# Optimization experiments

Hardware: AMD Instinct MI355X
Metric: run time of the kernel (lower is better)

## Reference

```python
import jax, jax.numpy as jnp
import numpy as np

B, S, D, H = 2, 2048, 1024, 16
HD = D // H  # 64


def setup_inputs() -> dict:
    key = jax.random.key(0)
    ks = jax.random.split(key, 7)
    s = 1.0 / np.sqrt(HD)
    return {
        "x": jax.random.normal(ks[0], (B, S, D), dtype=jnp.float32),
        "Wq": jax.random.normal(ks[1], (H, HD, HD), dtype=jnp.float32) * s,
        "bq": jax.random.normal(ks[2], (H, HD), dtype=jnp.float32) * 0.01,
        "Wk": jax.random.normal(ks[3], (H, HD, HD), dtype=jnp.float32) * s,
        "bk": jax.random.normal(ks[4], (H, HD), dtype=jnp.float32) * 0.01,
        "Wv": jax.random.normal(ks[5], (H, HD, HD), dtype=jnp.float32) * s,
        "bv": jax.random.normal(ks[6], (H, HD), dtype=jnp.float32) * 0.01,
    }


def reference(x, Wq, bq, Wk, bk, Wv, bv):
    b, s, d = x.shape
    h, hd, _ = Wq.shape
    # Faithful to torch: x.view(B, H, S, hd) is a raw reshape (mixes seq positions
    # across heads), NOT a transpose-based head split.
    xh = x.reshape(b, h, s, hd)
    # torch Linear: y @ W.T + b, with W of shape (out, in)
    q = jnp.einsum('bhse,hde->bhsd', xh, Wq) + bq[None, :, None, :]
    k = jnp.einsum('bhse,hde->bhsd', xh, Wk) + bk[None, :, None, :]
    v = jnp.einsum('bhse,hde->bhsd', xh, Wv) + bv[None, :, None, :]
    scale = 1.0 / jnp.sqrt(jnp.asarray(d / h, dtype=jnp.float32))
    attn = jax.nn.softmax(jnp.einsum('bhqd,bhkd->bhqk', q, k) * scale, axis=-1)
    out = jnp.einsum('bhqk,bhkd->bhqd', attn, v)
    # torch.cat over heads along last dim == transpose then merge
    return out.transpose(0, 2, 1, 3).reshape(b, s, d)
```

## Files before the change

### kernel.cpp

```cpp
#include <hip/hip_runtime.h>
#include <hip/hip_bf16.h>

#define BATCH 2
#define SEQ   2048
#define DMODEL 1024
#define NH    16
#define HD    64
#define QSCALE 0.1803368801111602f

typedef __attribute__((ext_vector_type(8))) short bf16x8;
typedef __attribute__((ext_vector_type(4))) float f32x4;

__device__ __forceinline__ ushort f2bf(float f) {
    union { float f; unsigned u; } v; v.f = f;
    return (ushort)((v.u + 0x8000u) >> 16);
}

__device__ __forceinline__ unsigned pack2bf(float a, float b) {
    union { float f; unsigned u; } x, y; x.f = a; y.f = b;
    return __builtin_amdgcn_perm(y.u + 0x8000u, x.u + 0x8000u, 0x07060302u);
}

__device__ __forceinline__ float exp2r(float x) {
#if __has_builtin(__builtin_amdgcn_exp2f)
    return __builtin_amdgcn_exp2f(x);
#else
    return exp2f(x);
#endif
}

__device__ __forceinline__ void g2l16(const void* g, void* l) {
    __builtin_amdgcn_global_load_lds(
        (const __attribute__((address_space(1))) unsigned*)g,
        (__attribute__((address_space(3))) unsigned*)l, 16, 0, 0);
}

#define MFMA(a, b, c) __builtin_amdgcn_mfma_f32_16x16x32_bf16((a), (b), (c), 0, 0, 0)

__global__ __launch_bounds__(256) void wfmt_kernel(
    const float* __restrict__ Wq, const float* __restrict__ Wk,
    const float* __restrict__ Wv, ushort* __restrict__ Wf)
{
    const int blk = blockIdx.x;
    const int h = blk / 3, m = blk - h * 3;
    const float* W = (m == 0 ? Wq : (m == 1 ? Wk : Wv)) + h * 4096;
    const float s = (m == 0) ? QSCALE : 1.0f;
    for (int i = 0; i < 2; ++i) {
        int idx = threadIdx.x + 256 * i;
        int l = idx & 63, chunk = idx >> 6;
        int qd = l >> 4, l16 = l & 15, nt = chunk >> 1, ks = chunk & 1;
        const float* src = W + (nt * 16 + l16) * 64 + ks * 32 + qd * 8;
        float4 a = *(const float4*)src;
        float4 b = *(const float4*)(src + 4);
        union { bf16x8 v; unsigned u[4]; } t;
        t.u[0] = pack2bf(a.x * s, a.y * s);
        t.u[1] = pack2bf(a.z * s, a.w * s);
        t.u[2] = pack2bf(b.x * s, b.y * s);
        t.u[3] = pack2bf(b.z * s, b.w * s);
        *(bf16x8*)&Wf[((size_t)blk * 512 + idx) * 8] = t.v;
    }
}

__global__ __launch_bounds__(256) void qkv_kernel(
    const float* __restrict__ x, const ushort* __restrict__ Wf,
    const float* __restrict__ bq, const float* __restrict__ bk,
    const float* __restrict__ bv,
    ushort* __restrict__ Qo, ushort* __restrict__ Kf, ushort* __restrict__ Vf)
{
    const int bid = blockIdx.x;
    const int st  = bid & 31;
    const int bh  = bid >> 5;
    const int h   = bh & (NH - 1);

    __shared__ ushort EbQ[64 * 72];
    __shared__ ushort EbK[64 * 72];
    __shared__ ushort EbV[64 * 72];

    const int tid  = threadIdx.x;
    const int wave = tid >> 6, lane = tid & 63;
    const int ln16 = lane & 15, quad = lane >> 4;

    const float* xr = x + (size_t)bh * (SEQ * HD)
                        + ((size_t)st * 64 + wave * 16 + ln16) * HD;
    bf16x8 afr[2];
#pragma unroll
    for (int ks = 0; ks < 2; ++ks) {
        const float4* p = (const float4*)(xr + ks * 32 + quad * 8);
        float4 a = p[0], b = p[1];
        union { bf16x8 v; unsigned u[4]; } t;
        t.u[0] = pack2bf(a.x, a.y);
        t.u[1] = pack2bf(a.z, a.w);
        t.u[2] = pack2bf(b.x, b.y);
        t.u[3] = pack2bf(b.z, b.w);
        afr[ks] = t.v;
    }

    const bf16x8* wf = (const bf16x8*)Wf + (size_t)h * 1536 + lane;

    f32x4 acc[3][4];
#pragma unroll
    for (int m = 0; m < 3; ++m)
#pragma unroll
        for (int nt = 0; nt < 4; ++nt) {
            f32x4 a = {0.f, 0.f, 0.f, 0.f};
            a = MFMA(afr[0], wf[(m * 8 + nt * 2 + 0) * 64], a);
            a = MFMA(afr[1], wf[(m * 8 + nt * 2 + 1) * 64], a);
            acc[m][nt] = a;
        }

#pragma unroll
    for (int nt = 0; nt < 4; ++nt) {
        float bbq = bq[h * 64 + nt * 16 + ln16] * QSCALE;
        float bbk = bk[h * 64 + nt * 16 + ln16];
#pragma unroll
        for (int r = 0; r < 4; ++r) {
            EbQ[(wave * 16 + quad * 4 + r) * 72 + nt * 16 + ln16] = f2bf(acc[0][nt][r] + bbq);
            EbK[(wave * 16 + quad * 4 + r) * 72 + nt * 16 + ln16] = f2bf(acc[1][nt][r] + bbk);
        }
        float bbv = bv[h * 64 + nt * 16 + ln16];
        ushort4 o;
        o.x = f2bf(acc[2][nt][0] + bbv);
        o.y = f2bf(acc[2][nt][1] + bbv);
        o.z = f2bf(acc[2][nt][2] + bbv);
        o.w = f2bf(acc[2][nt][3] + bbv);
        *(ushort4*)&EbV[(nt * 16 + ln16) * 72 + wave * 16 + quad * 4] = o;
    }
    __syncthreads();

    {
        ushort* dst = Qo + (size_t)bh * SEQ * HD + (size_t)st * 64 * HD;
        for (int i = 0; i < 2; ++i) {
            int idx = tid + 256 * i;
            int row = idx >> 3, c8 = (idx & 7) * 8;
            *(bf16x8*)&dst[row * 64 + c8] = *(const bf16x8*)&EbQ[row * 72 + c8];
        }
    }
    {
        ushort* dstK = Kf + ((size_t)bh * 32 + st) * 4096;
        ushort* dstV = Vf + ((size_t)bh * 32 + st) * 4096;
        for (int i = 0; i < 2; ++i) {
            int idx8 = tid + 256 * i;
            int l2 = idx8 & 63, chunk = idx8 >> 6;
            int nt = chunk >> 1, ks = chunk & 1;
            int qd = l2 >> 4, l16 = l2 & 15;
            *(bf16x8*)&dstK[(size_t)idx8 * 8] =
                *(const bf16x8*)&EbK[(nt * 16 + l16) * 72 + ks * 32 + qd * 8];
            *(bf16x8*)&dstV[(size_t)idx8 * 8] =
                *(const bf16x8*)&EbV[(nt * 16 + l16) * 72 + ks * 32 + qd * 8];
        }
    }
}

__global__ __launch_bounds__(256, 2) void attn_kernel(
    const ushort* __restrict__ Q, const ushort* __restrict__ Kf,
    const ushort* __restrict__ Vf, float* __restrict__ out)
{
    const int bid = blockIdx.x;
    const int wid = (bid & 7) * 64 + (bid >> 3);
    const int qt  = wid & 15;
    const int bh  = wid >> 4;
    const int h   = bh & (NH - 1), b = bh >> 4;

    __shared__ ushort Ksh[3][4096];
    __shared__ ushort Vsh[3][4096];
    __shared__ ushort Ps[4][2][2048];

    const int tid = threadIdx.x, wave = tid >> 6, lane = tid & 63;
    const int ln16 = lane & 15, quad = lane >> 4;
    const unsigned swz = (unsigned)(ln16 & 7) << 4;

    const char* kgb = (const char*)Kf + (size_t)bh * 32 * 8192 + wave * 2048 + lane * 16;
    const char* vgb = (const char*)Vf + (size_t)bh * 32 * 8192 + wave * 2048 + lane * 16;

    auto stage = [&](int kt, int sb) {
        const char* kg = kgb + (size_t)kt * 8192;
        const char* vg = vgb + (size_t)kt * 8192;
        ushort* kl = &Ksh[sb][wave * 1024];
        ushort* vl = &Vsh[sb][wave * 1024];
        g2l16(kg,        kl);
        g2l16(kg + 1024, kl + 512);
        g2l16(vg,        vl);
        g2l16(vg + 1024, vl + 512);
    };

    stage(0, 0);
    stage(1, 1);

    bf16x8 qfr[2][2];
#pragma unroll
    for (int g = 0; g < 2; ++g) {
        const ushort* Qg = Q + ((size_t)bh * SEQ + qt * 128 + wave * 32 + g * 16 + ln16) * HD;
        qfr[g][0] = *(const bf16x8*)&Qg[quad * 8];
        qfr[g][1] = *(const bf16x8*)&Qg[32 + quad * 8];
    }

    float lsum[2] = {0.f, 0.f};
    f32x4 accO[2][4];
#pragma unroll
    for (int g = 0; g < 2; ++g)
#pragma unroll
        for (int nt = 0; nt < 4; ++nt) accO[g][nt] = (f32x4){0.f, 0.f, 0.f, 0.f};

    bf16x8 vf[8];

    for (int kt = 0; kt < 32; ++kt) {
        const int cur = kt & 1;
        const int sb  = kt % 3;

        if (kt < 31) {
            asm volatile("s_waitcnt vmcnt(4)" ::: "memory");
        } else {
            asm volatile("s_waitcnt vmcnt(0)" ::: "memory");
        }
        __builtin_amdgcn_s_barrier();
        __builtin_amdgcn_sched_barrier(0);

        const ushort* Kb = &Ksh[sb][0];
        bf16x8 kf[8];
#pragma unroll
        for (int c = 0; c < 8; ++c) kf[c] = *(const bf16x8*)&Kb[c * 512 + lane * 8];

        f32x4 sacc[2][4];
        __builtin_amdgcn_s_setprio(1);
#pragma unroll
        for (int nt = 0; nt < 4; ++nt)
#pragma unroll
            for (int g = 0; g < 2; ++g) {
                f32x4 a = {0.f, 0.f, 0.f, 0.f};
                a = MFMA(kf[nt * 2],     qfr[g][0], a);
                a = MFMA(kf[nt * 2 + 1], qfr[g][1], a);
                sacc[g][nt] = a;
            }
        __builtin_amdgcn_s_setprio(0);

        if (kt > 0) {
            const char* Pr = (const char*)Ps[wave][1 - cur];
            bf16x8 pf[2][2];
#pragma unroll
            for (int g = 0; g < 2; ++g) {
                const char* Prr = Pr + (g * 16 + ln16) * 128;
                pf[g][0] = *(const bf16x8*)(Prr + (((unsigned)(quad * 16)) ^ swz));
                pf[g][1] = *(const bf16x8*)(Prr + (((unsigned)(64 + quad * 16)) ^ swz));
            }
            __builtin_amdgcn_s_setprio(1);
#pragma unroll
            for (int nt = 0; nt < 4; ++nt)
#pragma unroll
                for (int g = 0; g < 2; ++g) {
                    accO[g][nt] = MFMA(vf[nt * 2],     pf[g][0], accO[g][nt]);
                    accO[g][nt] = MFMA(vf[nt * 2 + 1], pf[g][1], accO[g][nt]);
                }
            __builtin_amdgcn_s_setprio(0);
        }

        const ushort* Vb = &Vsh[sb][0];
#pragma unroll
        for (int c = 0; c < 8; ++c) vf[c] = *(const bf16x8*)&Vb[c * 512 + lane * 8];

        char* Pw = (char*)Ps[wave][cur];
#pragma unroll
        for (int g = 0; g < 2; ++g) {
            char* Pwr = Pw + (g * 16 + ln16) * 128;
            float rs = 0.f;
#pragma unroll
            for (int nt = 0; nt < 4; ++nt) {
                float p0 = exp2r(sacc[g][nt][0]);
                float p1 = exp2r(sacc[g][nt][1]);
                float p2 = exp2r(sacc[g][nt][2]);
                float p3 = exp2r(sacc[g][nt][3]);
                rs += (p0 + p1) + (p2 + p3);
                uint2 pk;
                pk.x = pack2bf(p0, p1);
                pk.y = pack2bf(p2, p3);
                *(uint2*)(Pwr + (((unsigned)(nt * 32 + quad * 8)) ^ swz)) = pk;
            }
            lsum[g] += rs;
        }

        if (kt < 30) {
            asm volatile("s_waitcnt lgkmcnt(0)" ::: "memory");
            __builtin_amdgcn_sched_barrier(0);
            stage(kt + 2, (kt + 2) % 3);
        }
    }

    {
        const char* Pr = (const char*)Ps[wave][1];
        bf16x8 pf[2][2];
#pragma unroll
        for (int g = 0; g < 2; ++g) {
            const char* Prr = Pr + (g * 16 + ln16) * 128;
            pf[g][0] = *(const bf16x8*)(Prr + (((unsigned)(quad * 16)) ^ swz));
            pf[g][1] = *(const bf16x8*)(Prr + (((unsigned)(64 + quad * 16)) ^ swz));
        }
#pragma unroll
        for (int nt = 0; nt < 4; ++nt)
#pragma unroll
            for (int g = 0; g < 2; ++g) {
                accO[g][nt] = MFMA(vf[nt * 2],     pf[g][0], accO[g][nt]);
                accO[g][nt] = MFMA(vf[nt * 2 + 1], pf[g][1], accO[g][nt]);
            }
    }

#pragma unroll
    for (int g = 0; g < 2; ++g) {
        float l = lsum[g];
        l += __shfl_xor(l, 16, 64);
        l += __shfl_xor(l, 32, 64);
        float rinv = 1.0f / l;
        float* ob = out + ((size_t)b * SEQ + qt * 128 + wave * 32 + g * 16 + ln16) * DMODEL + h * HD;
#pragma unroll
        for (int nt = 0; nt < 4; ++nt) {
            float4 o;
            o.x = accO[g][nt][0] * rinv;
            o.y = accO[g][nt][1] * rinv;
            o.z = accO[g][nt][2] * rinv;
            o.w = accO[g][nt][3] * rinv;
            *(float4*)&ob[nt * 16 + quad * 4] = o;
        }
    }
}

extern "C" void kernel_launch(void* const* d_in, const int* in_sizes, int n_in,
                              void* d_out, int out_size, void* d_ws, size_t ws_size,
                              hipStream_t stream) {
    const float* x  = (const float*)d_in[0];
    const float* Wq = (const float*)d_in[1];
    const float* bq = (const float*)d_in[2];
    const float* Wk = (const float*)d_in[3];
    const float* bk = (const float*)d_in[4];
    const float* Wv = (const float*)d_in[5];
    const float* bv = (const float*)d_in[6];

    const size_t nElem = (size_t)BATCH * NH * SEQ * HD;
    ushort* Qw  = (ushort*)d_ws;
    ushort* Kw  = Qw + nElem;
    ushort* Vw  = Kw + nElem;
    ushort* Wfw = Vw + nElem;

    wfmt_kernel<<<48, 256, 0, stream>>>(Wq, Wk, Wv, Wfw);
    qkv_kernel<<<32 * 32, 256, 0, stream>>>(
        x, Wfw, bq, bk, bv, Qw, Kw, Vw);
    attn_kernel<<<BATCH * NH * (SEQ / 128), 256, 0, stream>>>(
        Qw, Kw, Vw, (float*)d_out);
}
```

Before: 132.5 us.

## Split attention KV range across two wave groups, load K/V directly to registers

The attention kernel now launches 512 threads per block. Two groups of four waves each process half of the 32 key tiles for the same query rows, and their partial outputs and row sums are combined through shared memory at the end. The LDS triple-buffered K/V staging with barriers is removed, and each wave loads K/V fragments straight from global memory into registers, prefetching the next K tile. This removes per-tile barriers and doubles parallelism per query tile. In exchange it relies on cache hits for repeated K/V reads across waves and adds a final reduction step.

```diff
diff --git a/kernel.cpp b/kernel.cpp
--- a/kernel.cpp
+++ b/kernel.cpp
@@ -27,12 +27,6 @@
 #else
     return exp2f(x);
 #endif
-}
-
-__device__ __forceinline__ void g2l16(const void* g, void* l) {
-    __builtin_amdgcn_global_load_lds(
-        (const __attribute__((address_space(1))) unsigned*)g,
-        (__attribute__((address_space(3))) unsigned*)l, 16, 0, 0);
 }
 
 #define MFMA(a, b, c) __builtin_amdgcn_mfma_f32_16x16x32_bf16((a), (b), (c), 0, 0, 0)
@@ -151,7 +145,7 @@
     }
 }
 
-__global__ __launch_bounds__(256, 2) void attn_kernel(
+__global__ __launch_bounds__(512, 4) void attn_kernel(
     const ushort* __restrict__ Q, const ushort* __restrict__ Kf,
     const ushort* __restrict__ Vf, float* __restrict__ out)
 {
@@ -161,39 +155,24 @@
     const int bh  = wid >> 4;
     const int h   = bh & (NH - 1), b = bh >> 4;
 
-    __shared__ ushort Ksh[3][4096];
-    __shared__ ushort Vsh[3][4096];
-    __shared__ ushort Ps[4][2][2048];
+    __shared__ ushort Ps[8][2][2048];
 
     const int tid = threadIdx.x, wave = tid >> 6, lane = tid & 63;
     const int ln16 = lane & 15, quad = lane >> 4;
+    const int qw = wave & 3, kh = wave >> 2;
     const unsigned swz = (unsigned)(ln16 & 7) << 4;
 
-    const char* kgb = (const char*)Kf + (size_t)bh * 32 * 8192 + wave * 2048 + lane * 16;
-    const char* vgb = (const char*)Vf + (size_t)bh * 32 * 8192 + wave * 2048 + lane * 16;
-
-    auto stage = [&](int kt, int sb) {
-        const char* kg = kgb + (size_t)kt * 8192;
-        const char* vg = vgb + (size_t)kt * 8192;
-        ushort* kl = &Ksh[sb][wave * 1024];
-        ushort* vl = &Vsh[sb][wave * 1024];
-        g2l16(kg,        kl);
-        g2l16(kg + 1024, kl + 512);
-        g2l16(vg,        vl);
-        g2l16(vg + 1024, vl + 512);
-    };
-
-    stage(0, 0);
-    stage(1, 1);
-
     bf16x8 qfr[2][2];
 #pragma unroll
     for (int g = 0; g < 2; ++g) {
-        const ushort* Qg = Q + ((size_t)bh * SEQ + qt * 128 + wave * 32 + g * 16 + ln16) * HD;
+        const ushort* Qg = Q + ((size_t)bh * SEQ + qt * 128 + qw * 32 + g * 16 + ln16) * HD;
         qfr[g][0] = *(const bf16x8*)&Qg[quad * 8];
         qfr[g][1] = *(const bf16x8*)&Qg[32 + quad * 8];
     }
 
+    const bf16x8* kfp = (const bf16x8*)(Kf + (size_t)bh * 32 * 4096) + kh * 8192 + lane;
+    const bf16x8* vfp = (const bf16x8*)(Vf + (size_t)bh * 32 * 4096) + kh * 8192 + lane;
+
     float lsum[2] = {0.f, 0.f};
     f32x4 accO[2][4];
 #pragma unroll
@@ -201,27 +180,15 @@
 #pragma unroll
         for (int nt = 0; nt < 4; ++nt) accO[g][nt] = (f32x4){0.f, 0.f, 0.f, 0.f};
 
-    bf16x8 vf[8];
-
-    for (int kt = 0; kt < 32; ++kt) {
+    bf16x8 kf[8], vf[8];
+#pragma unroll
+    for (int c = 0; c < 8; ++c) kf[c] = kfp[c * 64];
+    kfp += 512;
+
+    for (int kt = 0; kt < 16; ++kt) {
         const int cur = kt & 1;
-        const int sb  = kt % 3;
-
-        if (kt < 31) {
-            asm volatile("s_waitcnt vmcnt(4)" ::: "memory");
-        } else {
-            asm volatile("s_waitcnt vmcnt(0)" ::: "memory");
-        }
-        __builtin_amdgcn_s_barrier();
-        __builtin_amdgcn_sched_barrier(0);
-
-        const ushort* Kb = &Ksh[sb][0];
-        bf16x8 kf[8];
-#pragma unroll
-        for (int c = 0; c < 8; ++c) kf[c] = *(const bf16x8*)&Kb[c * 512 + lane * 8];
 
         f32x4 sacc[2][4];
-        __builtin_amdgcn_s_setprio(1);
 #pragma unroll
         for (int nt = 0; nt < 4; ++nt)
 #pragma unroll
@@ -231,7 +198,12 @@
                 a = MFMA(kf[nt * 2 + 1], qfr[g][1], a);
                 sacc[g][nt] = a;
             }
-        __builtin_amdgcn_s_setprio(0);
+
+        if (kt < 15) {
+#pragma unroll
+            for (int c = 0; c < 8; ++c) kf[c] = kfp[c * 64];
+            kfp += 512;
+        }
 
         if (kt > 0) {
             const char* Pr = (const char*)Ps[wave][1 - cur];
@@ -242,7 +214,6 @@
                 pf[g][0] = *(const bf16x8*)(Prr + (((unsigned)(quad * 16)) ^ swz));
                 pf[g][1] = *(const bf16x8*)(Prr + (((unsigned)(64 + quad * 16)) ^ swz));
             }
-            __builtin_amdgcn_s_setprio(1);
 #pragma unroll
             for (int nt = 0; nt < 4; ++nt)
 #pragma unroll
@@ -250,12 +221,11 @@
                     accO[g][nt] = MFMA(vf[nt * 2],     pf[g][0], accO[g][nt]);
                     accO[g][nt] = MFMA(vf[nt * 2 + 1], pf[g][1], accO[g][nt]);
                 }
-            __builtin_amdgcn_s_setprio(0);
-        }
-
-        const ushort* Vb = &Vsh[sb][0];
-#pragma unroll
-        for (int c = 0; c < 8; ++c) vf[c] = *(const bf16x8*)&Vb[c * 512 + lane * 8];
+        }
+
+#pragma unroll
+        for (int c = 0; c < 8; ++c) vf[c] = vfp[c * 64];
+        vfp += 512;
 
         char* Pw = (char*)Ps[wave][cur];
 #pragma unroll
@@ -276,12 +246,6 @@
             }
             lsum[g] += rs;
         }
-
-        if (kt < 30) {
-            asm volatile("s_waitcnt lgkmcnt(0)" ::: "memory");
-            __builtin_amdgcn_sched_barrier(0);
-            stage(kt + 2, (kt + 2) % 3);
-        }
     }
 
     {
@@ -302,21 +266,49 @@
             }
     }
 
-#pragma unroll
-    for (int g = 0; g < 2; ++g) {
-        float l = lsum[g];
-        l += __shfl_xor(l, 16, 64);
-        l += __shfl_xor(l, 32, 64);
-        float rinv = 1.0f / l;
-        float* ob = out + ((size_t)b * SEQ + qt * 128 + wave * 32 + g * 16 + ln16) * DMODEL + h * HD;
-#pragma unroll
-        for (int nt = 0; nt < 4; ++nt) {
-            float4 o;
-            o.x = accO[g][nt][0] * rinv;
-            o.y = accO[g][nt][1] * rinv;
-            o.z = accO[g][nt][2] * rinv;
-            o.w = accO[g][nt][3] * rinv;
-            *(float4*)&ob[nt * 16 + quad * 4] = o;
+    __syncthreads();
+    if (kh == 1) {
+        float* ex = (float*)&Ps[wave][0][0];
+#pragma unroll
+        for (int g = 0; g < 2; ++g)
+#pragma unroll
+            for (int nt = 0; nt < 4; ++nt)
+                *(f32x4*)&ex[((g * 4 + nt) * 64 + lane) * 4] = accO[g][nt];
+        float* exl = (float*)&Ps[wave - 4][0][0];
+        exl[lane * 2 + 0] = lsum[0];
+        exl[lane * 2 + 1] = lsum[1];
+    }
+    __syncthreads();
+    if (kh == 0) {
+        const float* ex  = (const float*)&Ps[wave + 4][0][0];
+        const float* exl = (const float*)&Ps[wave][0][0];
+#pragma unroll
+        for (int g = 0; g < 2; ++g)
+#pragma unroll
+            for (int nt = 0; nt < 4; ++nt) {
+                f32x4 o = *(const f32x4*)&ex[((g * 4 + nt) * 64 + lane) * 4];
+                accO[g][nt][0] += o[0]; accO[g][nt][1] += o[1];
+                accO[g][nt][2] += o[2]; accO[g][nt][3] += o[3];
+            }
+        lsum[0] += exl[lane * 2 + 0];
+        lsum[1] += exl[lane * 2 + 1];
+
+#pragma unroll
+        for (int g = 0; g < 2; ++g) {
+            float l = lsum[g];
+            l += __shfl_xor(l, 16, 64);
+            l += __shfl_xor(l, 32, 64);
+            float rinv = 1.0f / l;
+            float* ob = out + ((size_t)b * SEQ + qt * 128 + qw * 32 + g * 16 + ln16) * DMODEL + h * HD;
+#pragma unroll
+            for (int nt = 0; nt < 4; ++nt) {
+                float4 o;
+                o.x = accO[g][nt][0] * rinv;
+                o.y = accO[g][nt][1] * rinv;
+                o.z = accO[g][nt][2] * rinv;
+                o.w = accO[g][nt][3] * rinv;
+                *(float4*)&ob[nt * 16 + quad * 4] = o;
+            }
         }
     }
 }
@@ -341,6 +333,6 @@
     wfmt_kernel<<<48, 256, 0, stream>>>(Wq, Wk, Wv, Wfw);
     qkv_kernel<<<32 * 32, 256, 0, stream>>>(
         x, Wfw, bq, bk, bv, Qw, Kw, Vw);
-    attn_kernel<<<BATCH * NH * (SEQ / 128), 256, 0, stream>>>(
+    attn_kernel<<<BATCH * NH * (SEQ / 128), 512, 0, stream>>>(
         Qw, Kw, Vw, (float*)d_out);
 }
```

Measured after the change: 154.6 us. +16.7%, slower.
